# Kernel tuning notes

Measured on AMD Instinct MI355X. Metric: run time of the kernel, lower is better.

Reference implementation:

```python
import jax, jax.numpy as jnp
import numpy as np

K = 16          # neighbors per point
POINTNUM = 2048 # opt.pointnum
B, N = 8, 2048


def _knn_concat(x, k):
    """x: [B,N,C] -> [B,N,k,2C] = concat(center, k-nearest neighbor feats)."""
    sq = jnp.sum(x * x, axis=-1)                                   # [B,N]
    d2 = sq[:, :, None] + sq[:, None, :] - 2.0 * jnp.einsum('bnc,bmc->bnm', x, x)
    _, idx = jax.lax.top_k(-d2, k)                                 # [B,N,k]
    nbr = jax.vmap(lambda xb, ib: xb[ib])(x, idx)                  # [B,N,k,C]
    ctr = jnp.broadcast_to(x[:, :, None, :], nbr.shape)
    return jnp.concatenate([ctr, nbr], axis=-1)


def _lin(x, w, b):
    return x @ w + b


lrelu = jax.nn.leaky_relu  # default negative_slope=0.01 matches nn.LeakyReLU()


def setup_inputs() -> dict:
    key = jax.random.key(0)
    ks = jax.random.split(key, 20)

    def w(k_, fi, fo):
        return jax.random.normal(k_, (fi, fo), jnp.float32) / np.sqrt(fi)

    inp = {
        'x': jax.random.normal(ks[0], (B, N, 3), jnp.float32),
        'h1w1': w(ks[1], 6, 16),   'h1b1': jnp.zeros((16,), jnp.float32),
        'h1w2': w(ks[2], 16, 64),  'h1b2': jnp.zeros((64,), jnp.float32),
        'h1w3': w(ks[3], 64, 32),  'h1b3': jnp.zeros((32,), jnp.float32),
        'h2w1': w(ks[4], 64, 256), 'h2b1': jnp.zeros((256,), jnp.float32),
        'h2w2': w(ks[5], 256, 128),'h2b2': jnp.zeros((128,), jnp.float32),
        'h3w1': w(ks[6], 256, 128),'h3b1': jnp.zeros((128,), jnp.float32),
        'fc1w': w(ks[7], 128, 128),'fc1b': jnp.zeros((128,), jnp.float32),
        'fc2w': w(ks[8], 128, 128),'fc2b': jnp.zeros((128,), jnp.float32),
        'fc3w': w(ks[9], 128, POINTNUM * 3), 'fc3b': jnp.zeros((POINTNUM * 3,), jnp.float32),
    }
    return inp


def reference(x, h1w1, h1b1, h1w2, h1b2, h1w3, h1b3,
              h2w1, h2b1, h2w2, h2b2, h3w1, h3b1,
              fc1w, fc1b, fc2w, fc2b, fc3w, fc3b):
    # block 1: knn-concat [B,N,K,6] -> MLP(6,16,64,32) -> sum over K
    x1 = _knn_concat(x, K)
    h = lrelu(_lin(x1, h1w1, h1b1))
    h = lrelu(_lin(h, h1w2, h1b2))
    h = lrelu(_lin(h, h1w3, h1b3))
    x2 = jnp.sum(h, axis=2)                    # [B,N,32]
    # block 2: [B,N,K,64] -> MLP(64,256,128) -> sum over K
    x2 = _knn_concat(x2, K)
    h = lrelu(_lin(x2, h2w1, h2b1))
    h = lrelu(_lin(h, h2w2, h2b2))
    x3 = jnp.sum(h, axis=2)                    # [B,N,128]
    # block 3: [B,N,K,256] -> MLP(256,128) -> sum over K
    x3 = _knn_concat(x3, K)
    h = lrelu(_lin(x3, h3w1, h3b1))
    x4 = jnp.sum(h, axis=2)                    # [B,N,128]
    # global max pool over points
    x5 = jnp.max(x4, axis=1)                   # [B,128]
    x6 = lrelu(_lin(x5, fc1w, fc1b))
    x7 = lrelu(_lin(x6, fc2w, fc2b))
    x8 = _lin(x7, fc3w, fc3b)                  # [B, POINTNUM*3]
    return x8.reshape(x8.shape[0], POINTNUM, 3)
```

## Files before the change

kernel.cpp:

```cpp
#include <hip/hip_runtime.h>

#define KNB 16
#define BSZ 8
#define NPT 2048

typedef __attribute__((ext_vector_type(8))) short bf16x8;
typedef __attribute__((ext_vector_type(4))) float f32x4;

__device__ __forceinline__ float lrelu(float x) { return x >= 0.f ? x : 0.01f * x; }

__device__ __forceinline__ unsigned short bf16rne(float f) {
    union { float f; unsigned int u; } v; v.f = f;
    return (unsigned short)((v.u + 0x7FFFu + ((v.u >> 16) & 1u)) >> 16);
}

__device__ __forceinline__ float packkey(float d, int idx) {
    union { float f; unsigned int u; } v; v.f = d;
    v.u = (v.u & 0xFFFFF800u) | (unsigned int)idx;
    return v.f;
}

__device__ __forceinline__ void ceA(float& a, float& b) {
    const float lo = fminf(a, b), hi = fmaxf(a, b);
    a = lo; b = hi;
}

__device__ __forceinline__ void bsort16(float* c) {
#pragma unroll
    for (int k = 2; k <= 16; k <<= 1) {
#pragma unroll
        for (int j = k >> 1; j > 0; j >>= 1) {
#pragma unroll
            for (int i = 0; i < 16; ++i) {
                const int l = i ^ j;
                if (l > i) {
                    if ((i & k) == 0) ceA(c[i], c[l]);
                    else              ceA(c[l], c[i]);
                }
            }
        }
    }
}

__device__ __forceinline__ void merge16(float* L, const float* C) {
#pragma unroll
    for (int i = 0; i < 16; ++i) L[i] = fminf(L[i], C[15 - i]);
#pragma unroll
    for (int j = 8; j > 0; j >>= 1) {
#pragma unroll
        for (int i = 0; i < 16; ++i) {
            const int l = i ^ j;
            if (l > i) ceA(L[i], L[l]);
        }
    }
}

__device__ __forceinline__ void st16(float* dst, const float* L) {
#pragma unroll
    for (int c = 0; c < 4; ++c)
        *(f32x4*)(dst + c * 4) = (f32x4){L[c * 4], L[c * 4 + 1], L[c * 4 + 2], L[c * 4 + 3]};
}

__device__ __forceinline__ void ld16(float* L, const float* src) {
#pragma unroll
    for (int c = 0; c < 4; ++c) {
        const f32x4 v = *(const f32x4*)(src + c * 4);
        L[c * 4] = v[0]; L[c * 4 + 1] = v[1]; L[c * 4 + 2] = v[2]; L[c * 4 + 3] = v[3];
    }
}

__device__ __forceinline__ void xwave_merge_out(float (*sS)[20], int w, int lane,
                                                float* L, float* outp) {
    st16(sS[w * 64 + lane], L);
    __syncthreads();
    if ((w & 1) == 0) {
        float C[16];
        ld16(C, sS[(w + 1) * 64 + lane]);
        merge16(L, C);
        if (w == 2) st16(sS[2 * 64 + lane], L);
    }
    __syncthreads();
    if (w == 0) {
        float C[16];
        ld16(C, sS[2 * 64 + lane]);
        merge16(L, C);
        st16(outp, L);
    }
}

__global__ void wprep_kernel(const float* __restrict__ w, unsigned short* __restrict__ wt,
                             int K, int N) {
    int i = blockIdx.x * 256 + threadIdx.x;
    if (i < K * N) { int k = i / N, n = i - k * N; wt[n * K + k] = bf16rne(w[i]); }
}

__global__ void wprep_b1_kernel(const float* __restrict__ w1, const float* __restrict__ w2,
                                const float* __restrict__ w3,
                                unsigned short* __restrict__ w1a, unsigned short* __restrict__ w2a,
                                unsigned short* __restrict__ w3a) {
    int i = blockIdx.x * 256 + threadIdx.x;
    if (i < 512) {
        int n = i >> 5, k = i & 31;
        w1a[i] = (k < 6) ? bf16rne(w1[k * 16 + n]) : (unsigned short)0;
    } else if (i < 2560) {
        int j = i - 512, n = j >> 5, k = j & 31;
        w2a[j] = (k < 16) ? bf16rne(w2[k * 64 + n]) : (unsigned short)0;
    } else if (i < 4608) {
        int j = i - 2560, n = j >> 6, k = j & 63;
        w3a[j] = bf16rne(w3[k * 32 + n]);
    }
}

template<int C>
__global__ void norms16_kernel(const unsigned short* __restrict__ feat, float* __restrict__ out) {
    int gid = blockIdx.x * blockDim.x + threadIdx.x;
    if (gid < BSZ * NPT) {
        const unsigned short* p = feat + (size_t)gid * C;
        float s = 0.f;
#pragma unroll
        for (int c8 = 0; c8 < C / 8; ++c8) {
            const bf16x8 v = *(const bf16x8*)(p + c8 * 8);
#pragma unroll
            for (int j = 0; j < 8; ++j) {
                union { unsigned int u; float f; } t;
                t.u = ((unsigned int)(unsigned short)v[j]) << 16;
                s = fmaf(t.f, t.f, s);
            }
        }
        out[gid] = s;
    }
}

template<int C>
__global__ void norms_kernel(const float* __restrict__ feat, float* __restrict__ out) {
    int gid = blockIdx.x * blockDim.x + threadIdx.x;
    if (gid < BSZ * NPT) {
        const float* p = feat + (size_t)gid * C;
        float s = 0.f;
#pragma unroll
        for (int c = 0; c < C; ++c) s = fmaf(p[c], p[c], s);
        out[gid] = s;
    }
}

template<int JS>
__launch_bounds__(256, 3)
__global__ void knn3_kernel(const float* __restrict__ feat,
                            const float* __restrict__ norms,
                            float* __restrict__ cand) {
    constexpr int JL = NPT / JS;
    constexpr int JP = JL / 4;
    const int b = blockIdx.z, js = blockIdx.y, i0 = blockIdx.x * 64;
    const int t = threadIdx.x, w = t >> 6, lane = t & 63;
    const float* fb = feat + (size_t)b * NPT * 3;
    const float* nb = norms + (size_t)b * NPT;

    __shared__ __align__(16) float sS[256][20];

    float q0, q1, q2;
    { const float* qp = fb + (size_t)(i0 + lane) * 3; q0 = qp[0]; q1 = qp[1]; q2 = qp[2]; }

    float L[16];
#pragma unroll
    for (int u = 0; u < 16; ++u) L[u] = 3e38f;

    const int jbeg = js * JL + w * JP;
#pragma unroll 1
    for (int j0 = jbeg; j0 < jbeg + JP; j0 += 16) {
        float C[16];
#pragma unroll
        for (int u = 0; u < 16; ++u) {
            const int j = j0 + u;
            const float* pp = fb + (size_t)j * 3;
            C[u] = packkey(fmaf(-2.f, fmaf(q0, pp[0], fmaf(q1, pp[1], q2 * pp[2])), nb[j]), j);
        }
        bsort16(C);
        merge16(L, C);
    }
    float* o = cand + (((size_t)b * NPT + i0 + lane) * JS + js) * 16;
    xwave_merge_out(sS, w, lane, L, o);
}

template<int C, int JS>
__launch_bounds__(256, 3)
__global__ void knn_mfma_kernel(const unsigned short* __restrict__ fb16,
                                const float* __restrict__ norms,
                                float* __restrict__ cand) {
    constexpr int JL = NPT / JS;
    constexpr int KS = C / 32;
    const int b    = blockIdx.z;
    const int js   = blockIdx.y;
    const int i0   = blockIdx.x * 64;
    const int t    = threadIdx.x;
    const int w    = t >> 6;
    const int lane = t & 63;
    const int l15  = lane & 15;
    const int quad = lane >> 4;
    const unsigned short* fbb = fb16 + (size_t)b * NPT * C;
    const float* nb = norms + (size_t)b * NPT;

    __shared__ __align__(16) float sS[256][20];

    bf16x8 afr[KS * 4];
#pragma unroll
    for (int ks = 0; ks < KS; ++ks)
#pragma unroll
        for (int mi = 0; mi < 4; ++mi)
            afr[ks * 4 + mi] = *(const bf16x8*)(fbb + (size_t)(i0 + mi * 16 + l15) * C + ks * 32 + quad * 8);

    float L[16];
#pragma unroll
    for (int u = 0; u < 16; ++u) L[u] = 3e38f;

    const int jbeg = js * JL;
#pragma unroll 1
    for (int j0 = jbeg; j0 < jbeg + JL; j0 += 64) {
        f32x4 acc[4];
#pragma unroll
        for (int mi = 0; mi < 4; ++mi) acc[mi] = (f32x4){0.f, 0.f, 0.f, 0.f};
        const unsigned short* prow = fbb + (size_t)(j0 + w * 16 + l15) * C + quad * 8;
#pragma unroll
        for (int ks = 0; ks < KS; ++ks) {
            const bf16x8 bfr = *(const bf16x8*)(prow + ks * 32);
#pragma unroll
            for (int mi = 0; mi < 4; ++mi)
                acc[mi] = __builtin_amdgcn_mfma_f32_16x16x32_bf16(afr[ks * 4 + mi], bfr, acc[mi], 0, 0, 0);
        }
        const float nv  = nb[j0 + w * 16 + l15];
        const int  cidx = j0 + w * 16 + l15;
#pragma unroll
        for (int mi = 0; mi < 4; ++mi)
#pragma unroll
            for (int r = 0; r < 4; ++r)
                sS[w * 64 + mi * 16 + quad * 4 + r][l15] = packkey(fmaf(-2.f, acc[mi][r], nv), cidx);
        float Cb[16];
        ld16(Cb, sS[w * 64 + lane]);
        bsort16(Cb);
        merge16(L, Cb);
    }

    float* o = cand + (((size_t)b * NPT + i0 + lane) * JS + js) * 16;
    xwave_merge_out(sS, w, lane, L, o);
}

template<int JS>
__launch_bounds__(256)
__global__ void knn_merge_kernel(const float* __restrict__ cand, int* __restrict__ knn_out) {
    const int q = blockIdx.x * 256 + threadIdx.x;
    const float* pd = cand + (size_t)q * JS * 16;
    float L[16];
    ld16(L, pd);
#pragma unroll
    for (int s = 1; s < JS; ++s) {
        float C[16];
        ld16(C, pd + s * 16);
        merge16(L, C);
    }
    int* o = knn_out + (size_t)q * KNB;
#pragma unroll
    for (int u = 0; u < 16; ++u) {
        union { float f; unsigned int v; } z; z.f = L[u];
        o[u] = (int)(z.v & 2047u);
    }
}

__launch_bounds__(256, 3)
__global__ void block1_mfma_kernel(const float* __restrict__ x, const int* __restrict__ knn,
                                   const unsigned short* __restrict__ w1a, const float* __restrict__ b1,
                                   const unsigned short* __restrict__ w2a, const float* __restrict__ b2,
                                   const unsigned short* __restrict__ w3a, const float* __restrict__ b3,
                                   unsigned short* __restrict__ x2b) {
    const int w = threadIdx.x >> 6, lane = threadIdx.x & 63;
    const int l15 = lane & 15, quad = lane >> 4;

    const bf16x8 W1 = *(const bf16x8*)(w1a + l15 * 32 + quad * 8);
    bf16x8 W2[4];
#pragma unroll
    for (int nt = 0; nt < 4; ++nt)
        W2[nt] = *(const bf16x8*)(w2a + (nt * 16 + l15) * 32 + quad * 8);
    bf16x8 W3[2][2];
#pragma unroll
    for (int tt = 0; tt < 2; ++tt)
#pragma unroll
        for (int ks = 0; ks < 2; ++ks)
            W3[tt][ks] = *(const bf16x8*)(w3a + (tt * 16 + l15) * 64 + ks * 32 + quad * 8);
    float b1v[4], b2v[4][4], b3v[2][4];
#pragma unroll
    for (int r = 0; r < 4; ++r) b1v[r] = b1[quad * 4 + r];
#pragma unroll
    for (int nt = 0; nt < 4; ++nt)
#pragma unroll
        for (int r = 0; r < 4; ++r) b2v[nt][r] = b2[nt * 16 + quad * 4 + r];
#pragma unroll
    for (int tt = 0; tt < 2; ++tt)
#pragma unroll
        for (int r = 0; r < 4; ++r) b3v[tt][r] = b3[tt * 16 + quad * 4 + r];

    const int src0 = ((2 * quad) & 3) * 16 + l15;
    const int src1 = ((2 * quad + 1) & 3) * 16 + l15;
    const int ntsel = quad >> 1;

    const int p0 = blockIdx.x * 16 + w * 4;
#pragma unroll 2
    for (int pi = 0; pi < 4; ++pi) {
        const int p = p0 + pi, b = p >> 11, n = p & (NPT - 1);
        int d0 = 0, d1 = 0, d2 = 0;
        if (quad == 0) {
            const float* xc = x + ((size_t)b * NPT + n) * 3;
            const int jn = knn[(size_t)p * KNB + l15];
            const float* xn = x + ((size_t)b * NPT + jn) * 3;
            const unsigned s0 = bf16rne(xc[0]), s1 = bf16rne(xc[1]), s2 = bf16rne(xc[2]);
            const unsigned s3 = bf16rne(xn[0]), s4 = bf16rne(xn[1]), s5 = bf16rne(xn[2]);
            d0 = (int)(s0 | (s1 << 16));
            d1 = (int)(s2 | (s3 << 16));
            d2 = (int)(s4 | (s5 << 16));
        }
        union { int i[4]; bf16x8 v; } B1;
        B1.i[0] = d0; B1.i[1] = d1; B1.i[2] = d2; B1.i[3] = 0;
        const f32x4 a1 = __builtin_amdgcn_mfma_f32_16x16x32_bf16(W1, B1.v, (f32x4){0.f, 0.f, 0.f, 0.f}, 0, 0, 0);

        int h10, h11;
        {
            const unsigned t0 = bf16rne(lrelu(a1[0] + b1v[0]));
            const unsigned t1 = bf16rne(lrelu(a1[1] + b1v[1]));
            const unsigned t2 = bf16rne(lrelu(a1[2] + b1v[2]));
            const unsigned t3 = bf16rne(lrelu(a1[3] + b1v[3]));
            h10 = (int)(t0 | (t1 << 16));
            h11 = (int)(t2 | (t3 << 16));
        }
        union { int i[4]; bf16x8 v; } B2;
        {
            const int e0 = __shfl(h10, src0), e1 = __shfl(h11, src0);
            const int e2 = __shfl(h10, src1), e3 = __shfl(h11, src1);
            const bool val = quad < 2;
            B2.i[0] = val ? e0 : 0; B2.i[1] = val ? e1 : 0;
            B2.i[2] = val ? e2 : 0; B2.i[3] = val ? e3 : 0;
        }
        f32x4 a2[4];
#pragma unroll
        for (int nt = 0; nt < 4; ++nt)
            a2[nt] = __builtin_amdgcn_mfma_f32_16x16x32_bf16(W2[nt], B2.v, (f32x4){0.f, 0.f, 0.f, 0.f}, 0, 0, 0);
        int dpk[4][2];
#pragma unroll
        for (int nt = 0; nt < 4; ++nt) {
            const unsigned t0 = bf16rne(lrelu(a2[nt][0] + b2v[nt][0]));
            const unsigned t1 = bf16rne(lrelu(a2[nt][1] + b2v[nt][1]));
            const unsigned t2 = bf16rne(lrelu(a2[nt][2] + b2v[nt][2]));
            const unsigned t3 = bf16rne(lrelu(a2[nt][3] + b2v[nt][3]));
            dpk[nt][0] = (int)(t0 | (t1 << 16));
            dpk[nt][1] = (int)(t2 | (t3 << 16));
        }
        f32x4 a3[2] = { (f32x4){0.f, 0.f, 0.f, 0.f}, (f32x4){0.f, 0.f, 0.f, 0.f} };
#pragma unroll
        for (int ks = 0; ks < 2; ++ks) {
            union { int i[4]; bf16x8 v; } B3;
            const int a0l = __shfl(dpk[2 * ks][0], src0), a0h = __shfl(dpk[2 * ks + 1][0], src0);
            const int a1l = __shfl(dpk[2 * ks][1], src0), a1h = __shfl(dpk[2 * ks + 1][1], src0);
            const int a2l = __shfl(dpk[2 * ks][0], src1), a2h = __shfl(dpk[2 * ks + 1][0], src1);
            const int a3l = __shfl(dpk[2 * ks][1], src1), a3h = __shfl(dpk[2 * ks + 1][1], src1);
            B3.i[0] = ntsel ? a0h : a0l;
            B3.i[1] = ntsel ? a1h : a1l;
            B3.i[2] = ntsel ? a2h : a2l;
            B3.i[3] = ntsel ? a3h : a3l;
#pragma unroll
            for (int tt = 0; tt < 2; ++tt)
                a3[tt] = __builtin_amdgcn_mfma_f32_16x16x32_bf16(W3[tt][ks], B3.v, a3[tt], 0, 0, 0);
        }
#pragma unroll
        for (int tt = 0; tt < 2; ++tt) {
#pragma unroll
            for (int r = 0; r < 4; ++r) {
                float s = lrelu(a3[tt][r] + b3v[tt][r]);
                s += __shfl_xor(s, 1);
                s += __shfl_xor(s, 2);
                s += __shfl_xor(s, 4);
                s += __shfl_xor(s, 8);
                if (l15 == 0)
                    x2b[(size_t)p * 32 + tt * 16 + quad * 4 + r] = bf16rne(s);
            }
        }
    }
}

__launch_bounds__(256, 2)
__global__ void block2_fused_kernel(const unsigned short* __restrict__ x2b,
                                    const int* __restrict__ knn,
                                    const unsigned short* __restrict__ w1t,
                                    const float* __restrict__ b1,
                                    const unsigned short* __restrict__ w2t,
                                    const float* __restrict__ b2,
                                    unsigned short* __restrict__ x3b) {
    const int w    = threadIdx.x >> 6;
    const int lane = threadIdx.x & 63;
    const int l15  = lane & 15, quad = lane >> 4;
    __shared__ __align__(16) unsigned short sH1[8][16][264];

    bf16x8 B1[4][2];
#pragma unroll
    for (int nt2 = 0; nt2 < 4; ++nt2)
#pragma unroll
        for (int ks = 0; ks < 2; ++ks)
            B1[nt2][ks] = *(const bf16x8*)(w1t + (size_t)(w * 64 + nt2 * 16 + l15) * 64 + ks * 32 + quad * 8);
    bf16x8 B2[2][8];
#pragma unroll
    for (int nt2 = 0; nt2 < 2; ++nt2)
#pragma unroll
        for (int ks = 0; ks < 8; ++ks)
            B2[nt2][ks] = *(const bf16x8*)(w2t + (size_t)(w * 32 + nt2 * 16 + l15) * 256 + ks * 32 + quad * 8);
    float b1v[4];
#pragma unroll
    for (int nt2 = 0; nt2 < 4; ++nt2) b1v[nt2] = b1[w * 64 + nt2 * 16 + l15];
    float b2v[2];
#pragma unroll
    for (int nt2 = 0; nt2 < 2; ++nt2) b2v[nt2] = b2[w * 32 + nt2 * 16 + l15];

    const int p0 = blockIdx.x * 8;
    const unsigned short* xb = x2b + (size_t)(p0 >> 11) * NPT * 32;

    int nbrv[8];
#pragma unroll
    for (int pi = 0; pi < 8; ++pi) nbrv[pi] = knn[(size_t)(p0 + pi) * KNB + l15];

    bf16x8 a0[8], a1[8];
#pragma unroll
    for (int pi = 0; pi < 8; ++pi) {
        a0[pi] = *(const bf16x8*)(x2b + (size_t)(p0 + pi) * 32 + quad * 8);
        a1[pi] = *(const bf16x8*)(xb + (size_t)nbrv[pi] * 32 + quad * 8);
    }

#pragma unroll
    for (int pi = 0; pi < 8; ++pi) {
#pragma unroll
        for (int nt2 = 0; nt2 < 4; ++nt2) {
            f32x4 acc = (f32x4){0.f, 0.f, 0.f, 0.f};
            acc = __builtin_amdgcn_mfma_f32_16x16x32_bf16(a0[pi], B1[nt2][0], acc, 0, 0, 0);
            acc = __builtin_amdgcn_mfma_f32_16x16x32_bf16(a1[pi], B1[nt2][1], acc, 0, 0, 0);
#pragma unroll
            for (int r = 0; r < 4; ++r)
                sH1[pi][quad * 4 + r][w * 64 + nt2 * 16 + l15] = bf16rne(lrelu(acc[r] + b1v[nt2]));
        }
    }

    __syncthreads();

#pragma unroll
    for (int pi = 0; pi < 8; ++pi) {
        bf16x8 af[8];
#pragma unroll
        for (int ks = 0; ks < 8; ++ks)
            af[ks] = *(const bf16x8*)&sH1[pi][l15][ks * 32 + quad * 8];
#pragma unroll
        for (int nt2 = 0; nt2 < 2; ++nt2) {
            f32x4 acc = (f32x4){0.f, 0.f, 0.f, 0.f};
#pragma unroll
            for (int ks = 0; ks < 8; ++ks)
                acc = __builtin_amdgcn_mfma_f32_16x16x32_bf16(af[ks], B2[nt2][ks], acc, 0, 0, 0);
            float s = 0.f;
#pragma unroll
            for (int r = 0; r < 4; ++r) s += lrelu(acc[r] + b2v[nt2]);
            s += __shfl_xor(s, 16);
            s += __shfl_xor(s, 32);
            if (quad == 0) x3b[(size_t)(p0 + pi) * 128 + w * 32 + nt2 * 16 + l15] = bf16rne(s);
        }
    }
}

__launch_bounds__(256, 3)
__global__ void block3_fused_kernel(const unsigned short* __restrict__ x3b,
                                    const int* __restrict__ knn,
                                    const unsigned short* __restrict__ w3t,
                                    const float* __restrict__ bias,
                                    float* __restrict__ x4) {
    const int w    = threadIdx.x >> 6;
    const int lane = threadIdx.x & 63;
    const int l15  = lane & 15, quad = lane >> 4;

    bf16x8 B3[2][8];
#pragma unroll
    for (int nt2 = 0; nt2 < 2; ++nt2)
#pragma unroll
        for (int ks = 0; ks < 8; ++ks)
            B3[nt2][ks] = *(const bf16x8*)(w3t + (size_t)(w * 32 + nt2 * 16 + l15) * 256 + ks * 32 + quad * 8);
    float bv[2];
#pragma unroll
    for (int nt2 = 0; nt2 < 2; ++nt2) bv[nt2] = bias[w * 32 + nt2 * 16 + l15];

    const int p0 = blockIdx.x * 8;
    const unsigned short* xb = x3b + (size_t)(p0 >> 11) * NPT * 128;

    int nbrv[8];
#pragma unroll
    for (int pi = 0; pi < 8; ++pi) nbrv[pi] = knn[(size_t)(p0 + pi) * KNB + l15];

    auto LDAF = [&](bf16x8* af, int pi, int nbr) {
        const unsigned short* ctr = x3b + (size_t)(p0 + pi) * 128 + quad * 8;
        const unsigned short* nbp = xb + (size_t)nbr * 128 + quad * 8;
#pragma unroll
        for (int ks = 0; ks < 4; ++ks) af[ks] = *(const bf16x8*)(ctr + ks * 32);
#pragma unroll
        for (int ks = 0; ks < 4; ++ks) af[4 + ks] = *(const bf16x8*)(nbp + ks * 32);
    };
    auto CMP = [&](int p, const bf16x8* af) {
#pragma unroll
        for (int nt2 = 0; nt2 < 2; ++nt2) {
            f32x4 acc = (f32x4){0.f, 0.f, 0.f, 0.f};
#pragma unroll
            for (int ks = 0; ks < 8; ++ks)
                acc = __builtin_amdgcn_mfma_f32_16x16x32_bf16(af[ks], B3[nt2][ks], acc, 0, 0, 0);
            float s = 0.f;
#pragma unroll
            for (int r = 0; r < 4; ++r) s += lrelu(acc[r] + bv[nt2]);
            s += __shfl_xor(s, 16);
            s += __shfl_xor(s, 32);
            if (quad == 0) x4[(size_t)p * 128 + w * 32 + nt2 * 16 + l15] = s;
        }
    };

    bf16x8 afA[8], afB[8];
    LDAF(afA, 0, nbrv[0]);
#pragma unroll
    for (int pj = 0; pj < 4; ++pj) {
        LDAF(afB, 2 * pj + 1, nbrv[2 * pj + 1]);
        CMP(p0 + 2 * pj, afA);
        if (pj < 3) LDAF(afA, 2 * pj + 2, nbrv[2 * pj + 2]);
        CMP(p0 + 2 * pj + 1, afB);
    }
}

__launch_bounds__(128)
__global__ void maxpool_partial_kernel(const float* __restrict__ x4,
                                       float* __restrict__ part) {
    const int chunk = blockIdx.x, b = blockIdx.y, t = threadIdx.x;
    const float* xb = x4 + ((size_t)b * NPT + (size_t)chunk * 128) * 128;
    float m = -1e30f;
#pragma unroll 8
    for (int n = 0; n < 128; ++n) m = fmaxf(m, xb[(size_t)n * 128 + t]);
    part[((size_t)b * 16 + chunk) * 128 + t] = m;
}

__launch_bounds__(128)
__global__ void head2_kernel(const float* __restrict__ part,
                             const float* __restrict__ fc1w, const float* __restrict__ fc1b,
                             const float* __restrict__ fc2w, const float* __restrict__ fc2b,
                             const float* __restrict__ fc3w, const float* __restrict__ fc3b,
                             float* __restrict__ out) {
    const int g = blockIdx.x, b = blockIdx.y, t = threadIdx.x;
    __shared__ float s5[128], s6[128], s7[128];
    float m = -1e30f;
#pragma unroll
    for (int c = 0; c < 16; ++c)
        m = fmaxf(m, part[((size_t)b * 16 + c) * 128 + t]);
    s5[t] = m;
    __syncthreads();
    float a = fc1b[t];
#pragma unroll 4
    for (int i = 0; i < 128; ++i) a = fmaf(s5[i], fc1w[i * 128 + t], a);
    s6[t] = lrelu(a);
    __syncthreads();
    a = fc2b[t];
#pragma unroll 4
    for (int i = 0; i < 128; ++i) a = fmaf(s6[i], fc2w[i * 128 + t], a);
    s7[t] = lrelu(a);
    __syncthreads();
    const int o = g * 128 + t;
    float acc = fc3b[o];
#pragma unroll 4
    for (int i = 0; i < 128; ++i) acc = fmaf(s7[i], fc3w[(size_t)i * 6144 + o], acc);
    out[(size_t)b * 6144 + o] = acc;
}

extern "C" void kernel_launch(void* const* d_in, const int* in_sizes, int n_in,
                              void* d_out, int out_size, void* d_ws, size_t ws_size,
                              hipStream_t stream) {
    const float* x    = (const float*)d_in[0];
    const float* h1w1 = (const float*)d_in[1];
    const float* h1b1 = (const float*)d_in[2];
    const float* h1w2 = (const float*)d_in[3];
    const float* h1b2 = (const float*)d_in[4];
    const float* h1w3 = (const float*)d_in[5];
    const float* h1b3 = (const float*)d_in[6];
    const float* h2w1 = (const float*)d_in[7];
    const float* h2b1 = (const float*)d_in[8];
    const float* h2w2 = (const float*)d_in[9];
    const float* h2b2 = (const float*)d_in[10];
    const float* h3w1 = (const float*)d_in[11];
    const float* h3b1 = (const float*)d_in[12];
    const float* fc1w = (const float*)d_in[13];
    const float* fc1b = (const float*)d_in[14];
    const float* fc2w = (const float*)d_in[15];
    const float* fc2b = (const float*)d_in[16];
    const float* fc3w = (const float*)d_in[17];
    const float* fc3b = (const float*)d_in[18];

    float* ws = (float*)d_ws;
    unsigned short* x2b16 = (unsigned short*)ws;
    unsigned short* x3b16 = (unsigned short*)(ws + 262144);
    float* x4   = ws + 1310720;
    int*   idx  = (int*)(ws + 3407872);
    float* nrm  = ws + 3670016;
    float* part = ws + 3686400;
    unsigned short* w1t = (unsigned short*)(ws + 3702784);
    unsigned short* w2t = (unsigned short*)(ws + 3710976);
    unsigned short* w3t = (unsigned short*)(ws + 3727360);
    unsigned short* w1a = (unsigned short*)(ws + 3743744);
    unsigned short* w2a = (unsigned short*)(ws + 3744000);
    unsigned short* w3a = (unsigned short*)(ws + 3745024);
    float* cd   = ws + 3746048;
    float* out  = (float*)d_out;

    const dim3 kg(32, 4, 8);

    wprep_kernel<<<64, 256, 0, stream>>>(h2w1, w1t, 64, 256);
    wprep_kernel<<<128, 256, 0, stream>>>(h2w2, w2t, 256, 128);
    wprep_kernel<<<128, 256, 0, stream>>>(h3w1, w3t, 256, 128);
    wprep_b1_kernel<<<18, 256, 0, stream>>>(h1w1, h1w2, h1w3, w1a, w2a, w3a);

    norms_kernel<3><<<64, 256, 0, stream>>>(x, nrm);
    knn3_kernel<4><<<kg, 256, 0, stream>>>(x, nrm, cd);
    knn_merge_kernel<4><<<64, 256, 0, stream>>>(cd, idx);
    block1_mfma_kernel<<<1024, 256, 0, stream>>>(x, idx, w1a, h1b1, w2a, h1b2, w3a, h1b3, x2b16);

    norms16_kernel<32><<<64, 256, 0, stream>>>(x2b16, nrm);
    knn_mfma_kernel<32, 4><<<kg, 256, 0, stream>>>(x2b16, nrm, cd);
    knn_merge_kernel<4><<<64, 256, 0, stream>>>(cd, idx);
    block2_fused_kernel<<<BSZ * NPT / 8, 256, 0, stream>>>(x2b16, idx, w1t, h2b1, w2t, h2b2, x3b16);

    norms16_kernel<128><<<64, 256, 0, stream>>>(x3b16, nrm);
    knn_mfma_kernel<128, 4><<<kg, 256, 0, stream>>>(x3b16, nrm, cd);
    knn_merge_kernel<4><<<64, 256, 0, stream>>>(cd, idx);
    block3_fused_kernel<<<BSZ * NPT / 8, 256, 0, stream>>>(x3b16, idx, w3t, h3b1, x4);

    maxpool_partial_kernel<<<dim3(16, 8), 128, 0, stream>>>(x4, part);
    head2_kernel<<<dim3(48, 8), 128, 0, stream>>>(part, fc1w, fc1b, fc2w, fc2b,
                                                  fc3w, fc3b, out);
}
```

Baseline: 374.2 us.

## Increase grid parallelism across kNN, merge, block kernels and fuse small prep kernels

Merges the four weight-prep launches into one kernel. Folds the block-1 output norm computation into block1, which removes a separate norms pass. The kNN column split goes from 4 to 8 slices, merge blocks shrink to 64 threads, block1 handles 2 points per wave, and maxpool uses more chunks, all to raise occupancy on the small grids. Block2 now streams points through a double-buffered small LDS tile with a sync per point instead of staging all 8. These trade more candidate traffic and more barriers for extra parallelism and fewer launches.

```diff
diff --git a/kernel.cpp b/kernel.cpp
--- a/kernel.cpp
+++ b/kernel.cpp
@@ -88,46 +88,38 @@
     }
 }
 
-__global__ void wprep_kernel(const float* __restrict__ w, unsigned short* __restrict__ wt,
-                             int K, int N) {
-    int i = blockIdx.x * 256 + threadIdx.x;
-    if (i < K * N) { int k = i / N, n = i - k * N; wt[n * K + k] = bf16rne(w[i]); }
-}
-
-__global__ void wprep_b1_kernel(const float* __restrict__ w1, const float* __restrict__ w2,
-                                const float* __restrict__ w3,
-                                unsigned short* __restrict__ w1a, unsigned short* __restrict__ w2a,
-                                unsigned short* __restrict__ w3a) {
-    int i = blockIdx.x * 256 + threadIdx.x;
-    if (i < 512) {
-        int n = i >> 5, k = i & 31;
-        w1a[i] = (k < 6) ? bf16rne(w1[k * 16 + n]) : (unsigned short)0;
-    } else if (i < 2560) {
-        int j = i - 512, n = j >> 5, k = j & 31;
-        w2a[j] = (k < 16) ? bf16rne(w2[k * 64 + n]) : (unsigned short)0;
-    } else if (i < 4608) {
-        int j = i - 2560, n = j >> 6, k = j & 63;
-        w3a[j] = bf16rne(w3[k * 32 + n]);
-    }
-}
-
-template<int C>
-__global__ void norms16_kernel(const unsigned short* __restrict__ feat, float* __restrict__ out) {
-    int gid = blockIdx.x * blockDim.x + threadIdx.x;
-    if (gid < BSZ * NPT) {
-        const unsigned short* p = feat + (size_t)gid * C;
-        float s = 0.f;
-#pragma unroll
-        for (int c8 = 0; c8 < C / 8; ++c8) {
-            const bf16x8 v = *(const bf16x8*)(p + c8 * 8);
-#pragma unroll
-            for (int j = 0; j < 8; ++j) {
-                union { unsigned int u; float f; } t;
-                t.u = ((unsigned int)(unsigned short)v[j]) << 16;
-                s = fmaf(t.f, t.f, s);
-            }
-        }
-        out[gid] = s;
+__global__ void wprep_all_kernel(const float* __restrict__ h2w1, unsigned short* __restrict__ w1t,
+                                 const float* __restrict__ h2w2, unsigned short* __restrict__ w2t,
+                                 const float* __restrict__ h3w1, unsigned short* __restrict__ w3t,
+                                 const float* __restrict__ w1, const float* __restrict__ w2,
+                                 const float* __restrict__ w3,
+                                 unsigned short* __restrict__ w1a, unsigned short* __restrict__ w2a,
+                                 unsigned short* __restrict__ w3a) {
+    const int bid = blockIdx.x, tid = threadIdx.x;
+    if (bid < 64) {
+        int i = bid * 256 + tid;
+        int k = i >> 8, n = i & 255;
+        w1t[n * 64 + k] = bf16rne(h2w1[i]);
+    } else if (bid < 192) {
+        int i = (bid - 64) * 256 + tid;
+        int k = i >> 7, n = i & 127;
+        w2t[n * 256 + k] = bf16rne(h2w2[i]);
+    } else if (bid < 320) {
+        int i = (bid - 192) * 256 + tid;
+        int k = i >> 7, n = i & 127;
+        w3t[n * 256 + k] = bf16rne(h3w1[i]);
+    } else {
+        int i = (bid - 320) * 256 + tid;
+        if (i < 512) {
+            int n = i >> 5, k = i & 31;
+            w1a[i] = (k < 6) ? bf16rne(w1[k * 16 + n]) : (unsigned short)0;
+        } else if (i < 2560) {
+            int j = i - 512, n = j >> 5, k = j & 31;
+            w2a[j] = (k < 16) ? bf16rne(w2[k * 64 + n]) : (unsigned short)0;
+        } else if (i < 4608) {
+            int j = i - 2560, n = j >> 6, k = j & 63;
+            w3a[j] = bf16rne(w3[k * 32 + n]);
+        }
     }
 }
 
@@ -141,6 +133,26 @@
         for (int c = 0; c < C; ++c) s = fmaf(p[c], p[c], s);
         out[gid] = s;
     }
+}
+
+__global__ void norms16q_kernel(const unsigned short* __restrict__ feat, float* __restrict__ out) {
+    const int gid = blockIdx.x * 256 + threadIdx.x;
+    const int q = gid >> 2, prt = gid & 3;
+    const unsigned short* p = feat + (size_t)q * 128 + prt * 32;
+    float s = 0.f;
+#pragma unroll
+    for (int c8 = 0; c8 < 4; ++c8) {
+        const bf16x8 v = *(const bf16x8*)(p + c8 * 8);
+#pragma unroll
+        for (int j = 0; j < 8; ++j) {
+            union { unsigned int u; float f; } t;
+            t.u = ((unsigned int)(unsigned short)v[j]) << 16;
+            s = fmaf(t.f, t.f, s);
+        }
+    }
+    s += __shfl_xor(s, 1);
+    s += __shfl_xor(s, 2);
+    if (prt == 0) out[q] = s;
 }
 
 template<int JS>
@@ -244,9 +256,9 @@
 }
 
 template<int JS>
-__launch_bounds__(256)
+__launch_bounds__(64)
 __global__ void knn_merge_kernel(const float* __restrict__ cand, int* __restrict__ knn_out) {
-    const int q = blockIdx.x * 256 + threadIdx.x;
+    const int q = blockIdx.x * 64 + threadIdx.x;
     const float* pd = cand + (size_t)q * JS * 16;
     float L[16];
     ld16(L, pd);
@@ -269,7 +281,7 @@
                                    const unsigned short* __restrict__ w1a, const float* __restrict__ b1,
                                    const unsigned short* __restrict__ w2a, const float* __restrict__ b2,
                                    const unsigned short* __restrict__ w3a, const float* __restrict__ b3,
-                                   unsigned short* __restrict__ x2b) {
+                                   unsigned short* __restrict__ x2b, float* __restrict__ nrm) {
     const int w = threadIdx.x >> 6, lane = threadIdx.x & 63;
     const int l15 = lane & 15, quad = lane >> 4;
 
@@ -300,9 +312,9 @@
     const int src1 = ((2 * quad + 1) & 3) * 16 + l15;
     const int ntsel = quad >> 1;
 
-    const int p0 = blockIdx.x * 16 + w * 4;
+    const int p0 = blockIdx.x * 8 + w * 2;
 #pragma unroll 2
-    for (int pi = 0; pi < 4; ++pi) {
+    for (int pi = 0; pi < 2; ++pi) {
         const int p = p0 + pi, b = p >> 11, n = p & (NPT - 1);
         int d0 = 0, d1 = 0, d2 = 0;
         if (quad == 0) {
@@ -366,6 +378,7 @@
             for (int tt = 0; tt < 2; ++tt)
                 a3[tt] = __builtin_amdgcn_mfma_f32_16x16x32_bf16(W3[tt][ks], B3.v, a3[tt], 0, 0, 0);
         }
+        float na = 0.f;
 #pragma unroll
         for (int tt = 0; tt < 2; ++tt) {
 #pragma unroll
@@ -375,10 +388,14 @@
                 s += __shfl_xor(s, 2);
                 s += __shfl_xor(s, 4);
                 s += __shfl_xor(s, 8);
+                na = fmaf(s, s, na);
                 if (l15 == 0)
                     x2b[(size_t)p * 32 + tt * 16 + quad * 4 + r] = bf16rne(s);
             }
         }
+        na += __shfl_xor(na, 16);
+        na += __shfl_xor(na, 32);
+        if (lane == 0) nrm[p] = na;
     }
 }
 
@@ -393,7 +410,7 @@
     const int w    = threadIdx.x >> 6;
     const int lane = threadIdx.x & 63;
     const int l15  = lane & 15, quad = lane >> 4;
-    __shared__ __align__(16) unsigned short sH1[8][16][264];
+    __shared__ __align__(16) unsigned short sH1[2][16][264];
 
     bf16x8 B1[4][2];
 #pragma unroll
@@ -415,40 +432,26 @@
     for (int nt2 = 0; nt2 < 2; ++nt2) b2v[nt2] = b2[w * 32 + nt2 * 16 + l15];
 
     const int p0 = blockIdx.x * 8;
-    const unsigned short* xb = x2b + (size_t)(p0 >> 11) * NPT * 32;
-
-    int nbrv[8];
-#pragma unroll
-    for (int pi = 0; pi < 8; ++pi) nbrv[pi] = knn[(size_t)(p0 + pi) * KNB + l15];
-
-    bf16x8 a0[8], a1[8];
-#pragma unroll
+#pragma unroll 1
     for (int pi = 0; pi < 8; ++pi) {
-        a0[pi] = *(const bf16x8*)(x2b + (size_t)(p0 + pi) * 32 + quad * 8);
-        a1[pi] = *(const bf16x8*)(xb + (size_t)nbrv[pi] * 32 + quad * 8);
-    }
-
-#pragma unroll
-    for (int pi = 0; pi < 8; ++pi) {
+        const int p = p0 + pi, b = p >> 11, buf = pi & 1;
+        const int nbr = knn[(size_t)p * KNB + l15];
+        const bf16x8 a0 = *(const bf16x8*)(x2b + (size_t)p * 32 + quad * 8);
+        const bf16x8 a1 = *(const bf16x8*)(x2b + ((size_t)(b * NPT) + nbr) * 32 + quad * 8);
 #pragma unroll
         for (int nt2 = 0; nt2 < 4; ++nt2) {
             f32x4 acc = (f32x4){0.f, 0.f, 0.f, 0.f};
-            acc = __builtin_amdgcn_mfma_f32_16x16x32_bf16(a0[pi], B1[nt2][0], acc, 0, 0, 0);
-            acc = __builtin_amdgcn_mfma_f32_16x16x32_bf16(a1[pi], B1[nt2][1], acc, 0, 0, 0);
+            acc = __builtin_amdgcn_mfma_f32_16x16x32_bf16(a0, B1[nt2][0], acc, 0, 0, 0);
+            acc = __builtin_amdgcn_mfma_f32_16x16x32_bf16(a1, B1[nt2][1], acc, 0, 0, 0);
 #pragma unroll
             for (int r = 0; r < 4; ++r)
-                sH1[pi][quad * 4 + r][w * 64 + nt2 * 16 + l15] = bf16rne(lrelu(acc[r] + b1v[nt2]));
-        }
-    }
-
-    __syncthreads();
-
-#pragma unroll
-    for (int pi = 0; pi < 8; ++pi) {
+                sH1[buf][quad * 4 + r][w * 64 + nt2 * 16 + l15] = bf16rne(lrelu(acc[r] + b1v[nt2]));
+        }
+        __syncthreads();
         bf16x8 af[8];
 #pragma unroll
         for (int ks = 0; ks < 8; ++ks)
-            af[ks] = *(const bf16x8*)&sH1[pi][l15][ks * 32 + quad * 8];
+            af[ks] = *(const bf16x8*)&sH1[buf][l15][ks * 32 + quad * 8];
 #pragma unroll
         for (int nt2 = 0; nt2 < 2; ++nt2) {
             f32x4 acc = (f32x4){0.f, 0.f, 0.f, 0.f};
@@ -460,7 +463,7 @@
             for (int r = 0; r < 4; ++r) s += lrelu(acc[r] + b2v[nt2]);
             s += __shfl_xor(s, 16);
             s += __shfl_xor(s, 32);
-            if (quad == 0) x3b[(size_t)(p0 + pi) * 128 + w * 32 + nt2 * 16 + l15] = bf16rne(s);
+            if (quad == 0) x3b[(size_t)p * 128 + w * 32 + nt2 * 16 + l15] = bf16rne(s);
         }
     }
 }
@@ -531,11 +534,11 @@
 __global__ void maxpool_partial_kernel(const float* __restrict__ x4,
                                        float* __restrict__ part) {
     const int chunk = blockIdx.x, b = blockIdx.y, t = threadIdx.x;
-    const float* xb = x4 + ((size_t)b * NPT + (size_t)chunk * 128) * 128;
+    const float* xb = x4 + ((size_t)b * NPT + (size_t)chunk * 64) * 128;
     float m = -1e30f;
 #pragma unroll 8
-    for (int n = 0; n < 128; ++n) m = fmaxf(m, xb[(size_t)n * 128 + t]);
-    part[((size_t)b * 16 + chunk) * 128 + t] = m;
+    for (int n = 0; n < 64; ++n) m = fmaxf(m, xb[(size_t)n * 128 + t]);
+    part[((size_t)b * 32 + chunk) * 128 + t] = m;
 }
 
 __launch_bounds__(128)
@@ -548,8 +551,8 @@
     __shared__ float s5[128], s6[128], s7[128];
     float m = -1e30f;
 #pragma unroll
-    for (int c = 0; c < 16; ++c)
-        m = fmaxf(m, part[((size_t)b * 16 + c) * 128 + t]);
+    for (int c = 0; c < 32; ++c)
+        m = fmaxf(m, part[((size_t)b * 32 + c) * 128 + t]);
     s5[t] = m;
     __syncthreads();
     float a = fc1b[t];
@@ -596,41 +599,39 @@
     unsigned short* x2b16 = (unsigned short*)ws;
     unsigned short* x3b16 = (unsigned short*)(ws + 262144);
     float* x4   = ws + 1310720;
+    float* cd   = x4;
     int*   idx  = (int*)(ws + 3407872);
     float* nrm  = ws + 3670016;
-    float* part = ws + 3686400;
     unsigned short* w1t = (unsigned short*)(ws + 3702784);
     unsigned short* w2t = (unsigned short*)(ws + 3710976);
     unsigned short* w3t = (unsigned short*)(ws + 3727360);
     unsigned short* w1a = (unsigned short*)(ws + 3743744);
     unsigned short* w2a = (unsigned short*)(ws + 3744000);
     unsigned short* w3a = (unsigned short*)(ws + 3745024);
-    float* cd   = ws + 3746048;
+    float* part = ws + 3746048;
     float* out  = (float*)d_out;
 
-    const dim3 kg(32, 4, 8);
-
-    wprep_kernel<<<64, 256, 0, stream>>>(h2w1, w1t, 64, 256);
-    wprep_kernel<<<128, 256, 0, stream>>>(h2w2, w2t, 256, 128);
-    wprep_kernel<<<128, 256, 0, stream>>>(h3w1, w3t, 256, 128);
-    wprep_b1_kernel<<<18, 256, 0, stream>>>(h1w1, h1w2, h1w3, w1a, w2a, w3a);
+    const dim3 kg(32, 8, 8);
+
+    wprep_all_kernel<<<338, 256, 0, stream>>>(h2w1, w1t, h2w2, w2t, h3w1, w3t,
+                                              h1w1, h1w2, h1w3, w1a, w2a, w3a);
 
     norms_kernel<3><<<64, 256, 0, stream>>>(x, nrm);
-    knn3_kernel<4><<<kg, 256, 0, stream>>>(x, nrm, cd);
-    knn_merge_kernel<4><<<64, 256, 0, stream>>>(cd, idx);
-    block1_mfma_kernel<<<1024, 256, 0, stream>>>(x, idx, w1a, h1b1, w2a, h1b2, w3a, h1b3, x2b16);
-
-    norms16_kernel<32><<<64, 256, 0, stream>>>(x2b16, nrm);
-    knn_mfma_kernel<32, 4><<<kg, 256, 0, stream>>>(x2b16, nrm, cd);
-    knn_merge_kernel<4><<<64, 256, 0, stream>>>(cd, idx);
+    knn3_kernel<8><<<kg, 256, 0, stream>>>(x, nrm, cd);
+    knn_merge_kernel<8><<<256, 64, 0, stream>>>(cd, idx);
+    block1_mfma_kernel<<<2048, 256, 0, stream>>>(x, idx, w1a, h1b1, w2a, h1b2, w3a, h1b3,
+                                                 x2b16, nrm);
+
+    knn_mfma_kernel<32, 8><<<kg, 256, 0, stream>>>(x2b16, nrm, cd);
+    knn_merge_kernel<8><<<256, 64, 0, stream>>>(cd, idx);
     block2_fused_kernel<<<BSZ * NPT / 8, 256, 0, stream>>>(x2b16, idx, w1t, h2b1, w2t, h2b2, x3b16);
 
-    norms16_kernel<128><<<64, 256, 0, stream>>>(x3b16, nrm);
-    knn_mfma_kernel<128, 4><<<kg, 256, 0, stream>>>(x3b16, nrm, cd);
-    knn_merge_kernel<4><<<64, 256, 0, stream>>>(cd, idx);
+    norms16q_kernel<<<256, 256, 0, stream>>>(x3b16, nrm);
+    knn_mfma_kernel<128, 8><<<kg, 256, 0, stream>>>(x3b16, nrm, cd);
+    knn_merge_kernel<8><<<256, 64, 0, stream>>>(cd, idx);
     block3_fused_kernel<<<BSZ * NPT / 8, 256, 0, stream>>>(x3b16, idx, w3t, h3b1, x4);
 
-    maxpool_partial_kernel<<<dim3(16, 8), 128, 0, stream>>>(x4, part);
+    maxpool_partial_kernel<<<dim3(32, 8), 128, 0, stream>>>(x4, part);
     head2_kernel<<<dim3(48, 8), 128, 0, stream>>>(part, fc1w, fc1b, fc2w, fc2b,
                                                   fc3w, fc3b, out);
 }
```

Result: faster. 364.5 us (-2.6%).
